# Kernel tuning notes

Measured on AMD Instinct MI355X. Metric: run time of the kernel, lower is better.

Reference implementation:

```python
import jax, jax.numpy as jnp
import numpy as np

N_NODES = 50000   # batch_size * num_nodes
N_EDGES = 800000
D_IN = 128
D_OUT = 128


def setup_inputs() -> dict:
    key = jax.random.key(0)
    k1, k2, k3, k4 = jax.random.split(key, 4)
    x = jax.random.normal(k1, (N_NODES, D_IN), dtype=jnp.float32)
    edge_index = jax.random.randint(k2, (2, N_EDGES), 0, N_NODES, dtype=jnp.int64)
    W = jax.random.normal(k3, (D_OUT, D_IN), dtype=jnp.float32) * (1.0 / np.sqrt(D_IN))
    b = jax.random.normal(k4, (D_OUT,), dtype=jnp.float32) * 0.01
    return {"x": x, "edge_index": edge_index, "batch_size": 50, "num_nodes": 1000, "W": W, "b": b}


def reference(x, edge_index, batch_size, num_nodes, W, b):
    dim_size = batch_size * num_nodes
    row, col = edge_index[0], edge_index[1]
    # gather messages and segment-mean aggregate over destination rows
    msgs = x[col]                                   # [E, D_IN]
    summed = jax.ops.segment_sum(msgs, row, num_segments=dim_size)      # [N, D_IN]
    counts = jax.ops.segment_sum(jnp.ones((row.shape[0],), dtype=x.dtype), row,
                                 num_segments=dim_size)                 # [N]
    mean = summed / jnp.maximum(counts, 1.0)[:, None]                   # 0 for empty rows
    # linear projection (torch Linear: y = x @ W.T + b)
    return mean @ W.T + b
```

## Files before the change

### kernel.cpp

```cpp
#include <hip/hip_runtime.h>

#define D 128
#define BSHIFT 5
#define BCAP 1024
#define EPB_A 2048

typedef unsigned short ushort_t;
typedef unsigned int uint_t;
typedef __attribute__((ext_vector_type(8))) short short8_t;
typedef __attribute__((ext_vector_type(4))) float f32x4_t;
typedef __attribute__((ext_vector_type(4))) uint_t uint4_t;
typedef const __attribute__((address_space(1))) void* gas_cptr;
typedef __attribute__((address_space(3))) void* las_ptr;
typedef const __attribute__((address_space(3))) ushort_t* las_cushort;

__device__ __forceinline__ bool eidx_is64(const int* eidx) {
    int lane = threadIdx.x & 63;
    int probe = eidx[2 * lane + 1];
    return __ballot(probe != 0) == 0ULL;
}

__device__ __forceinline__ uint_t f2bf(float f) {
    union { float f; uint_t i; } v; v.f = f;
    return (v.i + 0x7fffu + ((v.i >> 16) & 1u)) >> 16;
}
__device__ __forceinline__ float bf_lo(uint_t w) {
    union { uint_t i; float f; } v; v.i = w << 16; return v.f;
}
__device__ __forceinline__ float bf_hi(uint_t w) {
    union { uint_t i; float f; } v; v.i = w & 0xffff0000u; return v.f;
}

__global__ __launch_bounds__(256) void pre_kernel(
    const int* __restrict__ eidx, int* __restrict__ gcur,
    int* __restrict__ bucket, int E, int NBUK, int ab,
    const float* __restrict__ x, uint_t* __restrict__ xb, int total8, int cvb,
    const float* __restrict__ Wsrc, uint_t* __restrict__ wb, int N) {
    int t = threadIdx.x;

    if ((int)blockIdx.x >= ab) {
        if (xb == nullptr) return;
        int cb = blockIdx.x - ab;
        if (cb < cvb) {
            int i = cb * 256 + t;
            if (i < total8) {
                const float4* p = (const float4*)(x + (size_t)i * 8);
                float4 a = p[0], b = p[1];
                uint4 o;
                o.x = f2bf(a.x) | (f2bf(a.y) << 16);
                o.y = f2bf(a.z) | (f2bf(a.w) << 16);
                o.z = f2bf(b.x) | (f2bf(b.y) << 16);
                o.w = f2bf(b.z) | (f2bf(b.w) << 16);
                *(uint4*)(xb + (size_t)i * 4) = o;
            }
            if (cb == 0 && t < 16) {
                uint4 z; z.x = 0u; z.y = 0u; z.z = 0u; z.w = 0u;
                ((uint4*)(xb + (size_t)N * (D / 2)))[t] = z;
            }
        } else {
            int i = (cb - cvb) * 256 + t;
            if (i < D * D / 8) {
                const float4* p = (const float4*)(Wsrc + (size_t)i * 8);
                float4 a = p[0], b = p[1];
                uint4 o;
                o.x = f2bf(a.x) | (f2bf(a.y) << 16);
                o.y = f2bf(a.z) | (f2bf(a.w) << 16);
                o.z = f2bf(b.x) | (f2bf(b.y) << 16);
                o.w = f2bf(b.z) | (f2bf(b.w) << 16);
                *(uint4*)(wb + (size_t)i * 4) = o;
            }
        }
        return;
    }

    __shared__ int lhist[2048];
    __shared__ int lbase[2048];
    bool is64 = eidx_is64(eidx);
    for (int i = t; i < NBUK; i += 256) lhist[i] = 0;
    __syncthreads();

    int e0 = blockIdx.x * EPB_A;
    int e1 = min(e0 + EPB_A, E);
    int rr[8], cc[8];
    #pragma unroll
    for (int k = 0; k < 8; ++k) {
        int e = e0 + t + k * 256;
        rr[k] = -1;
        if (e < e1) {
            if (is64) { rr[k] = eidx[2 * e]; cc[k] = eidx[2 * E + 2 * e]; }
            else      { rr[k] = eidx[e];     cc[k] = eidx[E + e]; }
            atomicAdd(&lhist[rr[k] >> BSHIFT], 1);
        }
    }
    __syncthreads();
    for (int i = t; i < NBUK; i += 256) {
        int h = lhist[i];
        lbase[i] = (h > 0) ? atomicAdd(&gcur[i], h) : 0;
        lhist[i] = 0;
    }
    __syncthreads();
    #pragma unroll
    for (int k = 0; k < 8; ++k) {
        if (rr[k] >= 0) {
            int b = rr[k] >> BSHIFT;
            int p = atomicAdd(&lhist[b], 1);
            int idx = lbase[b] + p;
            if (idx < BCAP) bucket[b * BCAP + idx] = ((rr[k] & 31) << 24) | cc[k];
        }
    }
}

#define ISSUE(c, bufsel)                                                      \
    {                                                                         \
        ushort_t* db_ = wstage + (bufsel) * 2048;                             \
        __builtin_amdgcn_global_load_lds(                                     \
            (gas_cptr)(xb + (size_t)(c).x * D + 8 * sl),                      \
            (las_ptr)(db_), 16, 0, 0);                                        \
        __builtin_amdgcn_global_load_lds(                                     \
            (gas_cptr)(xb + (size_t)(c).y * D + 8 * sl),                      \
            (las_ptr)(db_ + 512), 16, 0, 0);                                  \
        __builtin_amdgcn_global_load_lds(                                     \
            (gas_cptr)(xb + (size_t)(c).z * D + 8 * sl),                      \
            (las_ptr)(db_ + 1024), 16, 0, 0);                                 \
        __builtin_amdgcn_global_load_lds(                                     \
            (gas_cptr)(xb + (size_t)(c).w * D + 8 * sl),                      \
            (las_ptr)(db_ + 1536), 16, 0, 0);                                 \
    }

#define ACCV(v)                                                               \
    a0 += bf_lo((v)[0]); a1 += bf_hi((v)[0]);                                 \
    a2 += bf_lo((v)[1]); a3 += bf_hi((v)[1]);                                 \
    a4 += bf_lo((v)[2]); a5 += bf_hi((v)[2]);                                 \
    a6 += bf_lo((v)[3]); a7 += bf_hi((v)[3]);

#define CONSUME                                                               \
    {                                                                         \
        uint4_t v0, v1, v2, v3;                                               \
        asm volatile("ds_read_b128 %0, %1"             : "=v"(v0) : "v"(sbp));\
        asm volatile("ds_read_b128 %0, %1 offset:1024" : "=v"(v1) : "v"(sbp));\
        asm volatile("ds_read_b128 %0, %1 offset:2048" : "=v"(v2) : "v"(sbp));\
        asm volatile("ds_read_b128 %0, %1 offset:3072" : "=v"(v3) : "v"(sbp));\
        asm volatile("s_waitcnt lgkmcnt(0)" ::: "memory");                    \
        __builtin_amdgcn_sched_barrier(0);                                    \
        ACCV(v0) ACCV(v1) ACCV(v2) ACCV(v3)                                   \
    }

__global__ __launch_bounds__(256, 3) void fused_bf_kernel(
    const ushort_t* __restrict__ xb, const int* __restrict__ gcur,
    const int* __restrict__ bucket, const ushort_t* __restrict__ Wb,
    const float* __restrict__ bias, float* __restrict__ out, int N) {
    __shared__ alignas(16) int sE[1152];
    __shared__ int lcnt[32], lpos[32], lstart[32];
    __shared__ alignas(16) ushort_t sA[32 * 136];
    __shared__ alignas(16) ushort_t stage[16384];
    int t = threadIdx.x;
    int b = blockIdx.x;

    if (t < 32) { lcnt[t] = 0; lpos[t] = 0; }
    __syncthreads();
    int tot = min(gcur[b], BCAP);
    const int* bp = bucket + (size_t)b * BCAP;
    for (int i = t; i < tot; i += 256)
        atomicAdd(&lcnt[bp[i] >> 24], 1);
    __syncthreads();
    if (t == 0) {
        int run = 0;
        #pragma unroll
        for (int i = 0; i < 32; ++i) {
            lstart[i] = run;
            run += (lcnt[i] + 3) & ~3;
        }
    }
    __syncthreads();
    for (int i = t; i < tot; i += 256) {
        int v = bp[i];
        int rl = v >> 24;
        int p = atomicAdd(&lpos[rl], 1);
        int idx = lstart[rl] + p;
        if (idx < 1152) sE[idx] = v & 0xFFFFFF;
    }
    if (t < 32) {
        int c0 = lcnt[t];
        int pe = (c0 + 3) & ~3;
        for (int p = c0; p < pe; ++p) {
            int idx = lstart[t] + p;
            if (idx < 1152) sE[idx] = N;
        }
    }
    __syncthreads();

    int lane = t & 63, wave = t >> 6;
    int qi = t >> 4, sl = t & 15;
    int nbase = b << BSHIFT;
    ushort_t* wstage = stage + (wave << 12);

    #pragma unroll
    for (int quad = 0; quad < 2; ++quad) {
        int n = 2 * qi + quad;
        int nr = lcnt[n];
        int st = lstart[n];
        int trips = ((nr + 3) & ~3) >> 2;
        int wmax = trips;
        wmax = max(wmax, __shfl_xor(wmax, 16));
        wmax = max(wmax, __shfl_xor(wmax, 32));
        float a0 = 0.f, a1 = 0.f, a2 = 0.f, a3 = 0.f;
        float a4 = 0.f, a5 = 0.f, a6 = 0.f, a7 = 0.f;
        if (wmax > 0) {
            int4 c0 = (0 < trips) ? *(const int4*)(sE + st)
                                  : make_int4(N, N, N, N);
            ISSUE(c0, 0)
            __builtin_amdgcn_sched_barrier(0);
            for (int bt = 0; bt < wmax; ++bt) {
                int buf = bt & 1;
                if (bt + 1 < wmax) {
                    int4 cn = (bt + 1 < trips)
                        ? *(const int4*)(sE + st + 4 * (bt + 1))
                        : make_int4(N, N, N, N);
                    ISSUE(cn, buf ^ 1)
                    __builtin_amdgcn_sched_barrier(0);
                    asm volatile("s_waitcnt vmcnt(4)" ::: "memory");
                } else {
                    asm volatile("s_waitcnt vmcnt(0)" ::: "memory");
                }
                __builtin_amdgcn_sched_barrier(0);
                las_cushort sbp = (las_cushort)(wstage + buf * 2048 + lane * 8);
                CONSUME
            }
        }
        float inv = (nr > 0) ? 1.0f / (float)nr : 0.0f;
        uint4 pk;
        pk.x = f2bf(a0 * inv) | (f2bf(a1 * inv) << 16);
        pk.y = f2bf(a2 * inv) | (f2bf(a3 * inv) << 16);
        pk.z = f2bf(a4 * inv) | (f2bf(a5 * inv) << 16);
        pk.w = f2bf(a6 * inv) | (f2bf(a7 * inv) << 16);
        *(uint4*)(sA + n * 136 + 8 * sl) = pk;
    }
    __syncthreads();

    {
        int rt = wave & 1, jgrp = wave >> 1;
        int ml = lane & 15, kh = lane >> 4;
        short8_t afr[4];
        #pragma unroll
        for (int ks = 0; ks < 4; ++ks)
            afr[ks] = *(const short8_t*)(sA + (rt * 16 + ml) * 136 + ks * 32 + kh * 8);
        f32x4_t acc[4];
        #pragma unroll
        for (int q = 0; q < 4; ++q) acc[q] = (f32x4_t){0.f, 0.f, 0.f, 0.f};
        #pragma unroll
        for (int q = 0; q < 4; ++q) {
            int j = (jgrp * 4 + q) * 16 + ml;
            #pragma unroll
            for (int ks = 0; ks < 4; ++ks) {
                short8_t bfr = *(const short8_t*)(Wb + (size_t)j * D + ks * 32 + kh * 8);
                acc[q] = __builtin_amdgcn_mfma_f32_16x16x32_bf16(afr[ks], bfr, acc[q], 0, 0, 0);
            }
        }
        #pragma unroll
        for (int q = 0; q < 4; ++q) {
            int j = (jgrp * 4 + q) * 16 + ml;
            float bj = bias[j];
            #pragma unroll
            for (int r = 0; r < 4; ++r) {
                int gn = nbase + rt * 16 + kh * 4 + r;
                if (gn < N) out[(size_t)gn * D + j] = acc[q][r] + bj;
            }
        }
    }
}

__global__ __launch_bounds__(256) void prep_kernel(
    const int* __restrict__ gcur, const int* __restrict__ bucket,
    int* __restrict__ elist, int* __restrict__ cnt,
    int* __restrict__ start, int N, int NBUK) {
    __shared__ int lcnt[32], lpos[32], lstart[32];
    int t = threadIdx.x;
    int b = blockIdx.x;
    if (t < 32) { lcnt[t] = 0; lpos[t] = 0; }
    __syncthreads();
    int tot = min(gcur[b], BCAP);
    const int* bp = bucket + (size_t)b * BCAP;
    for (int i = t; i < tot; i += 256)
        atomicAdd(&lcnt[bp[i] >> 24], 1);
    __syncthreads();
    if (t == 0) {
        int run = 0;
        #pragma unroll
        for (int i = 0; i < 32; ++i) {
            lstart[i] = run;
            run += (lcnt[i] + 3) & ~3;
        }
    }
    __syncthreads();
    for (int i = t; i < tot; i += 256) {
        int v = bp[i];
        int rl = v >> 24;
        int p = atomicAdd(&lpos[rl], 1);
        int idx = lstart[rl] + p;
        if (idx < BCAP) elist[(size_t)b * BCAP + idx] = v & 0xFFFFFF;
    }
    if (t < 32) {
        int gr = (b << BSHIFT) + t;
        if (gr < N) { cnt[gr] = lcnt[t]; start[gr] = b * BCAP + lstart[t]; }
    }
}

__global__ __launch_bounds__(256, 6) void fused_kernel(
    const float* __restrict__ x, const int* __restrict__ elist,
    const int* __restrict__ cnt, const int* __restrict__ start,
    const float* __restrict__ W, const float* __restrict__ bias,
    float* __restrict__ out, int N) {
    __shared__ float sT[128 * 36];
    __shared__ float wc[16 * 132];
    int t = threadIdx.x;
    int lane = t & 63, wave = t >> 6;
    int half = lane >> 5, sl = lane & 31;
    int nbase = blockIdx.x * 32;

    #pragma unroll
    for (int pair = 0; pair < 4; ++pair) {
        int n = wave * 8 + pair * 2 + half;
        int gn = nbase + n;
        int nr  = (gn < N) ? cnt[gn]   : 0;
        int beg = (gn < N) ? start[gn] : 0;
        int nro  = __shfl(nr, lane ^ 32);
        int both = min(nr, nro);
        float ax = 0.f, ay = 0.f, az = 0.f, aw = 0.f;
        int i = 0;
        for (; i + 8 <= both; i += 8) {
            int4 cA = *(const int4*)(elist + beg + i);
            int4 cB = *(const int4*)(elist + beg + i + 4);
            float4 v0 = *(const float4*)(x + (size_t)cA.x * D + 4 * sl);
            float4 v1 = *(const float4*)(x + (size_t)cA.y * D + 4 * sl);
            float4 v2 = *(const float4*)(x + (size_t)cA.z * D + 4 * sl);
            float4 v3 = *(const float4*)(x + (size_t)cA.w * D + 4 * sl);
            float4 v4 = *(const float4*)(x + (size_t)cB.x * D + 4 * sl);
            float4 v5 = *(const float4*)(x + (size_t)cB.y * D + 4 * sl);
            float4 v6 = *(const float4*)(x + (size_t)cB.z * D + 4 * sl);
            float4 v7 = *(const float4*)(x + (size_t)cB.w * D + 4 * sl);
            ax += ((v0.x + v1.x) + (v2.x + v3.x)) + ((v4.x + v5.x) + (v6.x + v7.x));
            ay += ((v0.y + v1.y) + (v2.y + v3.y)) + ((v4.y + v5.y) + (v6.y + v7.y));
            az += ((v0.z + v1.z) + (v2.z + v3.z)) + ((v4.z + v5.z) + (v6.z + v7.z));
            aw += ((v0.w + v1.w) + (v2.w + v3.w)) + ((v4.w + v5.w) + (v6.w + v7.w));
        }
        for (; i < nr; ++i) {
            int c0 = elist[beg + i];
            float4 v = *(const float4*)(x + (size_t)c0 * D + 4 * sl);
            ax += v.x; ay += v.y; az += v.z; aw += v.w;
        }
        float inv = (nr > 0) ? 1.0f / (float)nr : 0.0f;
        int k0 = 4 * sl;
        sT[(k0 + 0) * 36 + n] = ax * inv;
        sT[(k0 + 1) * 36 + n] = ay * inv;
        sT[(k0 + 2) * 36 + n] = az * inv;
        sT[(k0 + 3) * 36 + n] = aw * inv;
    }

    int jg = t & 31, ng = t >> 5;
    int j0 = jg * 4, n0 = ng * 4;
    float acc[4][4] = {};
    for (int kc = 0; kc < 8; ++kc) {
        __syncthreads();
        #pragma unroll
        for (int i = 0; i < 8; ++i) {
            int idx = t + i * 256;
            int j = idx >> 4, kk = idx & 15;
            wc[kk * 132 + j] = W[j * D + kc * 16 + kk];
        }
        __syncthreads();
        #pragma unroll
        for (int kk = 0; kk < 16; ++kk) {
            int k = kc * 16 + kk;
            float4 s4 = *(const float4*)(sT + k * 36 + n0);
            float4 w4 = *(const float4*)(wc + kk * 132 + j0);
            acc[0][0] = fmaf(s4.x, w4.x, acc[0][0]); acc[0][1] = fmaf(s4.x, w4.y, acc[0][1]);
            acc[0][2] = fmaf(s4.x, w4.z, acc[0][2]); acc[0][3] = fmaf(s4.x, w4.w, acc[0][3]);
            acc[1][0] = fmaf(s4.y, w4.x, acc[1][0]); acc[1][1] = fmaf(s4.y, w4.y, acc[1][1]);
            acc[1][2] = fmaf(s4.y, w4.z, acc[1][2]); acc[1][3] = fmaf(s4.y, w4.w, acc[1][3]);
            acc[2][0] = fmaf(s4.z, w4.x, acc[2][0]); acc[2][1] = fmaf(s4.z, w4.y, acc[2][1]);
            acc[2][2] = fmaf(s4.z, w4.z, acc[2][2]); acc[2][3] = fmaf(s4.z, w4.w, acc[2][3]);
            acc[3][0] = fmaf(s4.w, w4.x, acc[3][0]); acc[3][1] = fmaf(s4.w, w4.y, acc[3][1]);
            acc[3][2] = fmaf(s4.w, w4.z, acc[3][2]); acc[3][3] = fmaf(s4.w, w4.w, acc[3][3]);
        }
    }
    float4 b4 = *(const float4*)(bias + j0);
    #pragma unroll
    for (int i = 0; i < 4; ++i) {
        int gn = nbase + n0 + i;
        if (gn >= N) continue;
        float4 o;
        o.x = acc[i][0] + b4.x;
        o.y = acc[i][1] + b4.y;
        o.z = acc[i][2] + b4.z;
        o.w = acc[i][3] + b4.w;
        *(float4*)(out + (size_t)gn * D + j0) = o;
    }
}

__global__ __launch_bounds__(256) void scatter_kernel(
    const float* __restrict__ x, const int* __restrict__ eidx,
    float* summed, float* __restrict__ counts, int E) {
    int t = blockIdx.x * 256 + threadIdx.x;
    int lane = threadIdx.x & 63;
    bool is64 = eidx_is64(eidx);
    int e = t >> 6;
    if (e >= E) return;
    int d = lane * 2;
    int r, c;
    if (is64) { r = eidx[2 * e]; c = eidx[2 * E + 2 * e]; }
    else      { r = eidx[e];     c = eidx[E + e]; }
    float2 v = *(const float2*)(x + (size_t)c * D + d);
    float* dst = summed + (size_t)r * D + d;
    atomicAdd(dst, v.x);
    atomicAdd(dst + 1, v.y);
    if (lane == 0) atomicAdd(counts + r, 1.0f);
}

__global__ __launch_bounds__(256) void divide_kernel(
    float* __restrict__ sums, const float* __restrict__ counts, int N) {
    int g = blockIdx.x * 256 + threadIdx.x;
    int r = g >> 6, lane = g & 63;
    if (r >= N) return;
    float inv = 1.0f / fmaxf(counts[r], 1.0f);
    float2* p = (float2*)(sums + (size_t)r * D + 2 * lane);
    float2 v = *p;
    v.x *= inv; v.y *= inv;
    *p = v;
}

__global__ __launch_bounds__(256) void gemm_kernel(
    float* inout, const float* __restrict__ W,
    const float* __restrict__ bias, int N) {
    __shared__ float sT[128 * 36];
    __shared__ float wc[32 * 132];
    int t = threadIdx.x;
    int nbase = blockIdx.x * 32;
    #pragma unroll
    for (int i = 0; i < 16; ++i) {
        int idx = t + i * 256;
        int n = idx >> 7, k = idx & 127;
        int gn = nbase + n;
        sT[k * 36 + n] = (gn < N) ? inout[(size_t)gn * D + k] : 0.0f;
    }
    int jg = t & 31, ng = t >> 5;
    int j0 = jg * 4, n0 = ng * 4;
    float acc[4][4] = {};
    for (int kc = 0; kc < 4; ++kc) {
        __syncthreads();
        #pragma unroll
        for (int i = 0; i < 16; ++i) {
            int idx = t + i * 256;
            int j = idx >> 5, kk = idx & 31;
            wc[kk * 132 + j] = W[j * D + kc * 32 + kk];
        }
        __syncthreads();
        #pragma unroll 8
        for (int kk = 0; kk < 32; ++kk) {
            int k = kc * 32 + kk;
            float4 s4 = *(const float4*)(sT + k * 36 + n0);
            float4 w4 = *(const float4*)(wc + kk * 132 + j0);
            acc[0][0] = fmaf(s4.x, w4.x, acc[0][0]); acc[0][1] = fmaf(s4.x, w4.y, acc[0][1]);
            acc[0][2] = fmaf(s4.x, w4.z, acc[0][2]); acc[0][3] = fmaf(s4.x, w4.w, acc[0][3]);
            acc[1][0] = fmaf(s4.y, w4.x, acc[1][0]); acc[1][1] = fmaf(s4.y, w4.y, acc[1][1]);
            acc[1][2] = fmaf(s4.y, w4.z, acc[1][2]); acc[1][3] = fmaf(s4.y, w4.w, acc[1][3]);
            acc[2][0] = fmaf(s4.z, w4.x, acc[2][0]); acc[2][1] = fmaf(s4.z, w4.y, acc[2][1]);
            acc[2][2] = fmaf(s4.z, w4.z, acc[2][2]); acc[2][3] = fmaf(s4.z, w4.w, acc[2][3]);
            acc[3][0] = fmaf(s4.w, w4.x, acc[3][0]); acc[3][1] = fmaf(s4.w, w4.y, acc[3][1]);
            acc[3][2] = fmaf(s4.w, w4.z, acc[3][2]); acc[3][3] = fmaf(s4.w, w4.w, acc[3][3]);
        }
    }
    float4 b4 = *(const float4*)(bias + j0);
    #pragma unroll
    for (int i = 0; i < 4; ++i) {
        int gn = nbase + n0 + i;
        if (gn >= N) continue;
        float4 o;
        o.x = acc[i][0] + b4.x;
        o.y = acc[i][1] + b4.y;
        o.z = acc[i][2] + b4.z;
        o.w = acc[i][3] + b4.w;
        *(float4*)(inout + (size_t)gn * D + j0) = o;
    }
}

extern "C" void kernel_launch(void* const* d_in, const int* in_sizes, int n_in,
                              void* d_out, int out_size, void* d_ws, size_t ws_size,
                              hipStream_t stream) {
    const float* x = (const float*)d_in[0];
    const int* eidx = (const int*)d_in[1];
    const float* W = (const float*)d_in[4];
    const float* b = (const float*)d_in[5];
    float* out = (float*)d_out;

    int N = in_sizes[0] / D;
    int E = in_sizes[1] / 2;
    int NBUK = (N + 31) >> BSHIFT;
    int ab = (E + EPB_A - 1) / EPB_A;

    size_t o0 = 0;
    size_t o_gc = o0;  o0 += ((size_t)NBUK * 4 + 255) & ~255ULL;
    size_t o_cn = o0;  o0 += ((size_t)N * 4 + 255) & ~255ULL;
    size_t o_st = o0;  o0 += ((size_t)N * 4 + 255) & ~255ULL;
    size_t o_bk = o0;  o0 += (size_t)NBUK * BCAP * 4;
    size_t o_el = o0;  o0 += (size_t)NBUK * BCAP * 4;
    size_t base_need = o0;
    size_t o_xb = o0;  o0 += (((size_t)(N + 1) * D * 2) + 255) & ~255ULL;
    size_t o_wb = o0;  size_t bf_need = o0 + (size_t)D * D * 2;

    bool cap_ok = (N <= 65536) && ((size_t)NBUK * BCAP >= (size_t)E);

    int cvb = (N * D / 8 + 255) / 256;
    int wvb = (D * D / 8 + 255) / 256;

    if (cap_ok && ws_size >= bf_need) {
        char* ws = (char*)d_ws;
        int*      gcur  = (int*)(ws + o_gc);
        int*      bkt   = (int*)(ws + o_bk);
        ushort_t* xb    = (ushort_t*)(ws + o_xb);
        ushort_t* wb    = (ushort_t*)(ws + o_wb);

        hipMemsetAsync(gcur, 0, (size_t)NBUK * 4, stream);
        pre_kernel<<<ab + cvb + wvb, 256, 0, stream>>>(
            eidx, gcur, bkt, E, NBUK, ab,
            x, (uint_t*)xb, N * D / 8, cvb, W, (uint_t*)wb, N);
        fused_bf_kernel<<<NBUK, 256, 0, stream>>>(xb, gcur, bkt, wb, b, out, N);
    } else if (cap_ok && ws_size >= base_need) {
        char* ws = (char*)d_ws;
        int* gcur  = (int*)(ws + o_gc);
        int* cnt   = (int*)(ws + o_cn);
        int* start = (int*)(ws + o_st);
        int* bkt   = (int*)(ws + o_bk);
        int* elist = (int*)(ws + o_el);
        int fb = (N + 31) / 32;

        hipMemsetAsync(gcur, 0, (size_t)NBUK * 4, stream);
        pre_kernel<<<ab, 256, 0, stream>>>(
            eidx, gcur, bkt, E, NBUK, ab,
            nullptr, nullptr, 0, 0, nullptr, nullptr, N);
        prep_kernel<<<NBUK, 256, 0, stream>>>(gcur, bkt, elist, cnt, start, N, NBUK);
        fused_kernel<<<fb, 256, 0, stream>>>(x, elist, cnt, start, W, b, out, N);
    } else {
        float* counts = (float*)d_ws;
        int fb = (N + 31) / 32;
        hipMemsetAsync(d_out, 0, (size_t)N * D * sizeof(float), stream);
        hipMemsetAsync(d_ws, 0, (size_t)N * sizeof(float), stream);
        int sb = (E * 64 + 255) / 256;
        scatter_kernel<<<sb, 256, 0, stream>>>(x, eidx, out, counts, E);
        int db = (N * 64 + 255) / 256;
        divide_kernel<<<db, 256, 0, stream>>>(out, counts, N);
        gemm_kernel<<<fb, 256, 0, stream>>>(out, W, b, N);
    }
}
```

Baseline: 157.8 us.

## Merge bucketing/convert and aggregate+GEMM into one persistent kernel with grid barrier

Replaces the two-kernel sequence (bucketing plus bf16 conversion, then fused aggregate+GEMM) with a single persistent kernel of fixed grid size. Blocks first loop over the bucketing and conversion tasks, then meet at a software grid barrier built on a global atomic counter, then loop over node buckets for the aggregation and MFMA projection. This removes one kernel launch and the gap between kernels, at the cost of a spin-wait barrier that needs all 768 blocks resident at once, plus the loss of the natural one-block-per-bucket scheduling.

```diff
diff --git a/kernel.cpp b/kernel.cpp
--- a/kernel.cpp
+++ b/kernel.cpp
@@ -4,6 +4,7 @@
 #define BSHIFT 5
 #define BCAP 1024
 #define EPB_A 2048
+#define GRID_MONO 768
 
 typedef unsigned short ushort_t;
 typedef unsigned int uint_t;
@@ -31,84 +32,6 @@
     union { uint_t i; float f; } v; v.i = w & 0xffff0000u; return v.f;
 }
 
-__global__ __launch_bounds__(256) void pre_kernel(
-    const int* __restrict__ eidx, int* __restrict__ gcur,
-    int* __restrict__ bucket, int E, int NBUK, int ab,
-    const float* __restrict__ x, uint_t* __restrict__ xb, int total8, int cvb,
-    const float* __restrict__ Wsrc, uint_t* __restrict__ wb, int N) {
-    int t = threadIdx.x;
-
-    if ((int)blockIdx.x >= ab) {
-        if (xb == nullptr) return;
-        int cb = blockIdx.x - ab;
-        if (cb < cvb) {
-            int i = cb * 256 + t;
-            if (i < total8) {
-                const float4* p = (const float4*)(x + (size_t)i * 8);
-                float4 a = p[0], b = p[1];
-                uint4 o;
-                o.x = f2bf(a.x) | (f2bf(a.y) << 16);
-                o.y = f2bf(a.z) | (f2bf(a.w) << 16);
-                o.z = f2bf(b.x) | (f2bf(b.y) << 16);
-                o.w = f2bf(b.z) | (f2bf(b.w) << 16);
-                *(uint4*)(xb + (size_t)i * 4) = o;
-            }
-            if (cb == 0 && t < 16) {
-                uint4 z; z.x = 0u; z.y = 0u; z.z = 0u; z.w = 0u;
-                ((uint4*)(xb + (size_t)N * (D / 2)))[t] = z;
-            }
-        } else {
-            int i = (cb - cvb) * 256 + t;
-            if (i < D * D / 8) {
-                const float4* p = (const float4*)(Wsrc + (size_t)i * 8);
-                float4 a = p[0], b = p[1];
-                uint4 o;
-                o.x = f2bf(a.x) | (f2bf(a.y) << 16);
-                o.y = f2bf(a.z) | (f2bf(a.w) << 16);
-                o.z = f2bf(b.x) | (f2bf(b.y) << 16);
-                o.w = f2bf(b.z) | (f2bf(b.w) << 16);
-                *(uint4*)(wb + (size_t)i * 4) = o;
-            }
-        }
-        return;
-    }
-
-    __shared__ int lhist[2048];
-    __shared__ int lbase[2048];
-    bool is64 = eidx_is64(eidx);
-    for (int i = t; i < NBUK; i += 256) lhist[i] = 0;
-    __syncthreads();
-
-    int e0 = blockIdx.x * EPB_A;
-    int e1 = min(e0 + EPB_A, E);
-    int rr[8], cc[8];
-    #pragma unroll
-    for (int k = 0; k < 8; ++k) {
-        int e = e0 + t + k * 256;
-        rr[k] = -1;
-        if (e < e1) {
-            if (is64) { rr[k] = eidx[2 * e]; cc[k] = eidx[2 * E + 2 * e]; }
-            else      { rr[k] = eidx[e];     cc[k] = eidx[E + e]; }
-            atomicAdd(&lhist[rr[k] >> BSHIFT], 1);
-        }
-    }
-    __syncthreads();
-    for (int i = t; i < NBUK; i += 256) {
-        int h = lhist[i];
-        lbase[i] = (h > 0) ? atomicAdd(&gcur[i], h) : 0;
-        lhist[i] = 0;
-    }
-    __syncthreads();
-    #pragma unroll
-    for (int k = 0; k < 8; ++k) {
-        if (rr[k] >= 0) {
-            int b = rr[k] >> BSHIFT;
-            int p = atomicAdd(&lhist[b], 1);
-            int idx = lbase[b] + p;
-            if (idx < BCAP) bucket[b * BCAP + idx] = ((rr[k] & 31) << 24) | cc[k];
-        }
-    }
-}
 
 #define ISSUE(c, bufsel)                                                      \
     {                                                                         \
@@ -145,126 +68,251 @@
         ACCV(v0) ACCV(v1) ACCV(v2) ACCV(v3)                                   \
     }
 
-__global__ __launch_bounds__(256, 3) void fused_bf_kernel(
-    const ushort_t* __restrict__ xb, const int* __restrict__ gcur,
-    const int* __restrict__ bucket, const ushort_t* __restrict__ Wb,
-    const float* __restrict__ bias, float* __restrict__ out, int N) {
+__global__ __launch_bounds__(256, 3) void mono_kernel(
+    const int* __restrict__ eidx, int* __restrict__ gcur,
+    int* __restrict__ bucket, const float* __restrict__ x,
+    ushort_t* __restrict__ xb, const float* __restrict__ Wsrc,
+    ushort_t* __restrict__ wb, const float* __restrict__ bias,
+    float* __restrict__ out, uint_t* __restrict__ bar,
+    int E, int N, int NBUK, int ab, int cvb, int wvb, int total8) {
+    __shared__ alignas(16) ushort_t stage[16384];
     __shared__ alignas(16) int sE[1152];
     __shared__ int lcnt[32], lpos[32], lstart[32];
     __shared__ alignas(16) ushort_t sA[32 * 136];
-    __shared__ alignas(16) ushort_t stage[16384];
     int t = threadIdx.x;
-    int b = blockIdx.x;
-
-    if (t < 32) { lcnt[t] = 0; lpos[t] = 0; }
-    __syncthreads();
-    int tot = min(gcur[b], BCAP);
-    const int* bp = bucket + (size_t)b * BCAP;
-    for (int i = t; i < tot; i += 256)
-        atomicAdd(&lcnt[bp[i] >> 24], 1);
+
+    int* lhist = (int*)stage;
+    int* lbase = (int*)(stage + 4096);
+    int ntask = ab + cvb + wvb;
+    for (int vt = blockIdx.x; vt < ntask; vt += gridDim.x) {
+        if (vt < ab) {
+            bool is64 = eidx_is64(eidx);
+            for (int i = t; i < NBUK; i += 256) lhist[i] = 0;
+            __syncthreads();
+            int e0 = vt * EPB_A;
+            int e1 = min(e0 + EPB_A, E);
+            int rr[8], cc[8];
+            #pragma unroll
+            for (int k = 0; k < 8; ++k) {
+                int e = e0 + t + k * 256;
+                rr[k] = -1;
+                if (e < e1) {
+                    if (is64) { rr[k] = eidx[2 * e]; cc[k] = eidx[2 * E + 2 * e]; }
+                    else      { rr[k] = eidx[e];     cc[k] = eidx[E + e]; }
+                    atomicAdd(&lhist[rr[k] >> BSHIFT], 1);
+                }
+            }
+            __syncthreads();
+            for (int i = t; i < NBUK; i += 256) {
+                int h = lhist[i];
+                lbase[i] = (h > 0) ? atomicAdd(&gcur[i], h) : 0;
+                lhist[i] = 0;
+            }
+            __syncthreads();
+            #pragma unroll
+            for (int k = 0; k < 8; ++k) {
+                if (rr[k] >= 0) {
+                    int b = rr[k] >> BSHIFT;
+                    int p = atomicAdd(&lhist[b], 1);
+                    int idx = lbase[b] + p;
+                    if (idx < BCAP) bucket[b * BCAP + idx] = ((rr[k] & 31) << 24) | cc[k];
+                }
+            }
+            __syncthreads();
+        } else if (vt < ab + cvb) {
+            int cb = vt - ab;
+            int i = cb * 256 + t;
+            if (i < total8) {
+                const float4* p = (const float4*)(x + (size_t)i * 8);
+                float4 a = p[0], b = p[1];
+                uint4 o;
+                o.x = f2bf(a.x) | (f2bf(a.y) << 16);
+                o.y = f2bf(a.z) | (f2bf(a.w) << 16);
+                o.z = f2bf(b.x) | (f2bf(b.y) << 16);
+                o.w = f2bf(b.z) | (f2bf(b.w) << 16);
+                *(uint4*)((uint_t*)xb + (size_t)i * 4) = o;
+            }
+            if (cb == 0 && t < 16) {
+                uint4 z; z.x = 0u; z.y = 0u; z.z = 0u; z.w = 0u;
+                ((uint4*)(xb + (size_t)N * D))[t] = z;
+            }
+        } else {
+            int i = (vt - ab - cvb) * 256 + t;
+            if (i < D * D / 8) {
+                const float4* p = (const float4*)(Wsrc + (size_t)i * 8);
+                float4 a = p[0], b = p[1];
+                uint4 o;
+                o.x = f2bf(a.x) | (f2bf(a.y) << 16);
+                o.y = f2bf(a.z) | (f2bf(a.w) << 16);
+                o.z = f2bf(b.x) | (f2bf(b.y) << 16);
+                o.w = f2bf(b.z) | (f2bf(b.w) << 16);
+                *(uint4*)((uint_t*)wb + (size_t)i * 4) = o;
+            }
+        }
+    }
+
+    __threadfence();
     __syncthreads();
     if (t == 0) {
-        int run = 0;
-        #pragma unroll
-        for (int i = 0; i < 32; ++i) {
-            lstart[i] = run;
-            run += (lcnt[i] + 3) & ~3;
-        }
-    }
-    __syncthreads();
-    for (int i = t; i < tot; i += 256) {
-        int v = bp[i];
-        int rl = v >> 24;
-        int p = atomicAdd(&lpos[rl], 1);
-        int idx = lstart[rl] + p;
-        if (idx < 1152) sE[idx] = v & 0xFFFFFF;
-    }
-    if (t < 32) {
-        int c0 = lcnt[t];
-        int pe = (c0 + 3) & ~3;
-        for (int p = c0; p < pe; ++p) {
-            int idx = lstart[t] + p;
-            if (idx < 1152) sE[idx] = N;
-        }
+        __hip_atomic_fetch_add(bar, 1u, __ATOMIC_RELEASE, __HIP_MEMORY_SCOPE_AGENT);
+        while (__hip_atomic_load(bar, __ATOMIC_ACQUIRE, __HIP_MEMORY_SCOPE_AGENT)
+               < (uint_t)gridDim.x)
+            __builtin_amdgcn_s_sleep(8);
     }
     __syncthreads();
 
     int lane = t & 63, wave = t >> 6;
     int qi = t >> 4, sl = t & 15;
-    int nbase = b << BSHIFT;
     ushort_t* wstage = stage + (wave << 12);
-
+    const ushort_t* Wb = wb;
+
+    for (int buk = blockIdx.x; buk < NBUK; buk += gridDim.x) {
+        if (t < 32) { lcnt[t] = 0; lpos[t] = 0; }
+        __syncthreads();
+        int tot = min(gcur[buk], BCAP);
+        const int* bp = bucket + (size_t)buk * BCAP;
+        for (int i = t; i < tot; i += 256)
+            atomicAdd(&lcnt[bp[i] >> 24], 1);
+        __syncthreads();
+        if (t == 0) {
+            int run = 0;
+            #pragma unroll
+            for (int i = 0; i < 32; ++i) {
+                lstart[i] = run;
+                run += (lcnt[i] + 3) & ~3;
+            }
+        }
+        __syncthreads();
+        for (int i = t; i < tot; i += 256) {
+            int v = bp[i];
+            int rl = v >> 24;
+            int p = atomicAdd(&lpos[rl], 1);
+            int idx = lstart[rl] + p;
+            if (idx < 1152) sE[idx] = v & 0xFFFFFF;
+        }
+        if (t < 32) {
+            int c0 = lcnt[t];
+            int pe = (c0 + 3) & ~3;
+            for (int p = c0; p < pe; ++p) {
+                int idx = lstart[t] + p;
+                if (idx < 1152) sE[idx] = N;
+            }
+        }
+        __syncthreads();
+
+        int nbase = buk << BSHIFT;
+        #pragma unroll
+        for (int quad = 0; quad < 2; ++quad) {
+            int n = 2 * qi + quad;
+            int nr = lcnt[n];
+            int st = lstart[n];
+            int trips = ((nr + 3) & ~3) >> 2;
+            int wmax = trips;
+            wmax = max(wmax, __shfl_xor(wmax, 16));
+            wmax = max(wmax, __shfl_xor(wmax, 32));
+            float a0 = 0.f, a1 = 0.f, a2 = 0.f, a3 = 0.f;
+            float a4 = 0.f, a5 = 0.f, a6 = 0.f, a7 = 0.f;
+            if (wmax > 0) {
+                int4 c0 = (0 < trips) ? *(const int4*)(sE + st)
+                                      : make_int4(N, N, N, N);
+                ISSUE(c0, 0)
+                __builtin_amdgcn_sched_barrier(0);
+                for (int bt = 0; bt < wmax; ++bt) {
+                    int buf = bt & 1;
+                    if (bt + 1 < wmax) {
+                        int4 cn = (bt + 1 < trips)
+                            ? *(const int4*)(sE + st + 4 * (bt + 1))
+                            : make_int4(N, N, N, N);
+                        ISSUE(cn, buf ^ 1)
+                        __builtin_amdgcn_sched_barrier(0);
+                        asm volatile("s_waitcnt vmcnt(4)" ::: "memory");
+                    } else {
+                        asm volatile("s_waitcnt vmcnt(0)" ::: "memory");
+                    }
+                    __builtin_amdgcn_sched_barrier(0);
+                    las_cushort sbp = (las_cushort)(wstage + buf * 2048 + lane * 8);
+                    CONSUME
+                }
+            }
+            float inv = (nr > 0) ? 1.0f / (float)nr : 0.0f;
+            uint4 pk;
+            pk.x = f2bf(a0 * inv) | (f2bf(a1 * inv) << 16);
+            pk.y = f2bf(a2 * inv) | (f2bf(a3 * inv) << 16);
+            pk.z = f2bf(a4 * inv) | (f2bf(a5 * inv) << 16);
+            pk.w = f2bf(a6 * inv) | (f2bf(a7 * inv) << 16);
+            *(uint4*)(sA + n * 136 + 8 * sl) = pk;
+        }
+        __syncthreads();
+
+        {
+            int rt = wave & 1, jgrp = wave >> 1;
+            int ml = lane & 15, kh = lane >> 4;
+            short8_t afr[4];
+            #pragma unroll
+            for (int ks = 0; ks < 4; ++ks)
+                afr[ks] = *(const short8_t*)(sA + (rt * 16 + ml) * 136 + ks * 32 + kh * 8);
+            f32x4_t acc[4];
+            #pragma unroll
+            for (int q = 0; q < 4; ++q) acc[q] = (f32x4_t){0.f, 0.f, 0.f, 0.f};
+            #pragma unroll
+            for (int q = 0; q < 4; ++q) {
+                int j = (jgrp * 4 + q) * 16 + ml;
+                #pragma unroll
+                for (int ks = 0; ks < 4; ++ks) {
+                    short8_t bfr = *(const short8_t*)(Wb + (size_t)j * D + ks * 32 + kh * 8);
+                    acc[q] = __builtin_amdgcn_mfma_f32_16x16x32_bf16(afr[ks], bfr, acc[q], 0, 0, 0);
+                }
+            }
+            #pragma unroll
+            for (int q = 0; q < 4; ++q) {
+                int j = (jgrp * 4 + q) * 16 + ml;
+                float bj = bias[j];
+                #pragma unroll
+                for (int r = 0; r < 4; ++r) {
+                    int gn = nbase + rt * 16 + kh * 4 + r;
+                    if (gn < N) out[(size_t)gn * D + j] = acc[q][r] + bj;
+                }
+            }
+        }
+    }
+}
+
+__global__ __launch_bounds__(256) void pre_kernel(
+    const int* __restrict__ eidx, int* __restrict__ gcur,
+    int* __restrict__ bucket, int E, int NBUK) {
+    __shared__ int lhist[2048];
+    __shared__ int lbase[2048];
+    bool is64 = eidx_is64(eidx);
+    int t = threadIdx.x;
+    for (int i = t; i < NBUK; i += 256) lhist[i] = 0;
+    __syncthreads();
+    int e0 = blockIdx.x * EPB_A;
+    int e1 = min(e0 + EPB_A, E);
+    int rr[8], cc[8];
     #pragma unroll
-    for (int quad = 0; quad < 2; ++quad) {
-        int n = 2 * qi + quad;
-        int nr = lcnt[n];
-        int st = lstart[n];
-        int trips = ((nr + 3) & ~3) >> 2;
-        int wmax = trips;
-        wmax = max(wmax, __shfl_xor(wmax, 16));
-        wmax = max(wmax, __shfl_xor(wmax, 32));
-        float a0 = 0.f, a1 = 0.f, a2 = 0.f, a3 = 0.f;
-        float a4 = 0.f, a5 = 0.f, a6 = 0.f, a7 = 0.f;
-        if (wmax > 0) {
-            int4 c0 = (0 < trips) ? *(const int4*)(sE + st)
-                                  : make_int4(N, N, N, N);
-            ISSUE(c0, 0)
-            __builtin_amdgcn_sched_barrier(0);
-            for (int bt = 0; bt < wmax; ++bt) {
-                int buf = bt & 1;
-                if (bt + 1 < wmax) {
-                    int4 cn = (bt + 1 < trips)
-                        ? *(const int4*)(sE + st + 4 * (bt + 1))
-                        : make_int4(N, N, N, N);
-                    ISSUE(cn, buf ^ 1)
-                    __builtin_amdgcn_sched_barrier(0);
-                    asm volatile("s_waitcnt vmcnt(4)" ::: "memory");
-                } else {
-                    asm volatile("s_waitcnt vmcnt(0)" ::: "memory");
-                }
-                __builtin_amdgcn_sched_barrier(0);
-                las_cushort sbp = (las_cushort)(wstage + buf * 2048 + lane * 8);
-                CONSUME
-            }
-        }
-        float inv = (nr > 0) ? 1.0f / (float)nr : 0.0f;
-        uint4 pk;
-        pk.x = f2bf(a0 * inv) | (f2bf(a1 * inv) << 16);
-        pk.y = f2bf(a2 * inv) | (f2bf(a3 * inv) << 16);
-        pk.z = f2bf(a4 * inv) | (f2bf(a5 * inv) << 16);
-        pk.w = f2bf(a6 * inv) | (f2bf(a7 * inv) << 16);
-        *(uint4*)(sA + n * 136 + 8 * sl) = pk;
-    }
-    __syncthreads();
-
-    {
-        int rt = wave & 1, jgrp = wave >> 1;
-        int ml = lane & 15, kh = lane >> 4;
-        short8_t afr[4];
-        #pragma unroll
-        for (int ks = 0; ks < 4; ++ks)
-            afr[ks] = *(const short8_t*)(sA + (rt * 16 + ml) * 136 + ks * 32 + kh * 8);
-        f32x4_t acc[4];
-        #pragma unroll
-        for (int q = 0; q < 4; ++q) acc[q] = (f32x4_t){0.f, 0.f, 0.f, 0.f};
-        #pragma unroll
-        for (int q = 0; q < 4; ++q) {
-            int j = (jgrp * 4 + q) * 16 + ml;
-            #pragma unroll
-            for (int ks = 0; ks < 4; ++ks) {
-                short8_t bfr = *(const short8_t*)(Wb + (size_t)j * D + ks * 32 + kh * 8);
-                acc[q] = __builtin_amdgcn_mfma_f32_16x16x32_bf16(afr[ks], bfr, acc[q], 0, 0, 0);
-            }
-        }
-        #pragma unroll
-        for (int q = 0; q < 4; ++q) {
-            int j = (jgrp * 4 + q) * 16 + ml;
-            float bj = bias[j];
-            #pragma unroll
-            for (int r = 0; r < 4; ++r) {
-                int gn = nbase + rt * 16 + kh * 4 + r;
-                if (gn < N) out[(size_t)gn * D + j] = acc[q][r] + bj;
-            }
+    for (int k = 0; k < 8; ++k) {
+        int e = e0 + t + k * 256;
+        rr[k] = -1;
+        if (e < e1) {
+            if (is64) { rr[k] = eidx[2 * e]; cc[k] = eidx[2 * E + 2 * e]; }
+            else      { rr[k] = eidx[e];     cc[k] = eidx[E + e]; }
+            atomicAdd(&lhist[rr[k] >> BSHIFT], 1);
+        }
+    }
+    __syncthreads();
+    for (int i = t; i < NBUK; i += 256) {
+        int h = lhist[i];
+        lbase[i] = (h > 0) ? atomicAdd(&gcur[i], h) : 0;
+        lhist[i] = 0;
+    }
+    __syncthreads();
+    #pragma unroll
+    for (int k = 0; k < 8; ++k) {
+        if (rr[k] >= 0) {
+            int b = rr[k] >> BSHIFT;
+            int p = atomicAdd(&lhist[b], 1);
+            int idx = lbase[b] + p;
+            if (idx < BCAP) bucket[b * BCAP + idx] = ((rr[k] & 31) << 24) | cc[k];
         }
     }
 }
@@ -498,7 +546,7 @@
     int ab = (E + EPB_A - 1) / EPB_A;
 
     size_t o0 = 0;
-    size_t o_gc = o0;  o0 += ((size_t)NBUK * 4 + 255) & ~255ULL;
+    size_t o_gc = o0;  o0 += ((size_t)NBUK * 4 + 4 + 255) & ~255ULL;
     size_t o_cn = o0;  o0 += ((size_t)N * 4 + 255) & ~255ULL;
     size_t o_st = o0;  o0 += ((size_t)N * 4 + 255) & ~255ULL;
     size_t o_bk = o0;  o0 += (size_t)NBUK * BCAP * 4;
@@ -515,15 +563,15 @@
     if (cap_ok && ws_size >= bf_need) {
         char* ws = (char*)d_ws;
         int*      gcur  = (int*)(ws + o_gc);
+        uint_t*   bar   = (uint_t*)(ws + o_gc + (size_t)NBUK * 4);
         int*      bkt   = (int*)(ws + o_bk);
         ushort_t* xb    = (ushort_t*)(ws + o_xb);
         ushort_t* wb    = (ushort_t*)(ws + o_wb);
 
-        hipMemsetAsync(gcur, 0, (size_t)NBUK * 4, stream);
-        pre_kernel<<<ab + cvb + wvb, 256, 0, stream>>>(
-            eidx, gcur, bkt, E, NBUK, ab,
-            x, (uint_t*)xb, N * D / 8, cvb, W, (uint_t*)wb, N);
-        fused_bf_kernel<<<NBUK, 256, 0, stream>>>(xb, gcur, bkt, wb, b, out, N);
+        hipMemsetAsync(gcur, 0, (size_t)NBUK * 4 + 4, stream);
+        mono_kernel<<<GRID_MONO, 256, 0, stream>>>(
+            eidx, gcur, bkt, x, xb, W, wb, b, out, bar,
+            E, N, NBUK, ab, cvb, wvb, N * D / 8);
     } else if (cap_ok && ws_size >= base_need) {
         char* ws = (char*)d_ws;
         int* gcur  = (int*)(ws + o_gc);
@@ -534,9 +582,7 @@
         int fb = (N + 31) / 32;
 
         hipMemsetAsync(gcur, 0, (size_t)NBUK * 4, stream);
-        pre_kernel<<<ab, 256, 0, stream>>>(
-            eidx, gcur, bkt, E, NBUK, ab,
-            nullptr, nullptr, 0, 0, nullptr, nullptr, N);
+        pre_kernel<<<ab, 256, 0, stream>>>(eidx, gcur, bkt, E, NBUK);
         prep_kernel<<<NBUK, 256, 0, stream>>>(gcur, bkt, elist, cnt, start, N, NBUK);
         fused_kernel<<<fb, 256, 0, stream>>>(x, elist, cnt, start, W, b, out, N);
     } else {
```

After: 370.2 us. 135% more time.

## Triple-buffer gather staging and vectorize edge/bucket index loads

Applied to the files above, without the earlier changes.

Extends the per-wave LDS staging used for the neighbour gather from a double buffer to a triple buffer, so two batches of row loads stay in flight while one is accumulated. The added LDS lowers the occupancy target from 3 to 2 blocks per CU. The bucketing pass now loads each thread's 8 contiguous edge indices with int4 loads instead of strided scalar loads. The fused kernel reads its bucket entries once with a vector load into registers, then reuses them for both the count and scatter passes. Giving up occupancy for deeper prefetch may not pay off if latency was already hidden.

```diff
diff --git a/kernel.cpp b/kernel.cpp
--- a/kernel.cpp
+++ b/kernel.cpp
@@ -81,17 +81,47 @@
 
     int e0 = blockIdx.x * EPB_A;
     int e1 = min(e0 + EPB_A, E);
+    int base = e0 + 8 * t;
     int rr[8], cc[8];
     #pragma unroll
-    for (int k = 0; k < 8; ++k) {
-        int e = e0 + t + k * 256;
-        rr[k] = -1;
-        if (e < e1) {
-            if (is64) { rr[k] = eidx[2 * e]; cc[k] = eidx[2 * E + 2 * e]; }
-            else      { rr[k] = eidx[e];     cc[k] = eidx[E + e]; }
-            atomicAdd(&lhist[rr[k] >> BSHIFT], 1);
-        }
-    }
+    for (int k = 0; k < 8; ++k) rr[k] = -1;
+    if (is64) {
+        if (base + 8 <= e1 && (E & 1) == 0) {
+            const int4* rp = (const int4*)(eidx + 2 * (size_t)base);
+            const int4* cp = (const int4*)(eidx + 2 * (size_t)E + 2 * (size_t)base);
+            #pragma unroll
+            for (int g = 0; g < 4; ++g) {
+                int4 r = rp[g], c = cp[g];
+                rr[2 * g]     = r.x; cc[2 * g]     = c.x;
+                rr[2 * g + 1] = r.z; cc[2 * g + 1] = c.z;
+            }
+        } else {
+            #pragma unroll
+            for (int k = 0; k < 8; ++k) {
+                int e = base + k;
+                if (e < e1) { rr[k] = eidx[2 * e]; cc[k] = eidx[2 * E + 2 * e]; }
+            }
+        }
+    } else {
+        if (base + 8 <= e1 && (E & 3) == 0) {
+            const int4* rp = (const int4*)(eidx + base);
+            const int4* cp = (const int4*)(eidx + (size_t)E + base);
+            int4 r0 = rp[0], r1 = rp[1], c0 = cp[0], c1 = cp[1];
+            rr[0] = r0.x; rr[1] = r0.y; rr[2] = r0.z; rr[3] = r0.w;
+            rr[4] = r1.x; rr[5] = r1.y; rr[6] = r1.z; rr[7] = r1.w;
+            cc[0] = c0.x; cc[1] = c0.y; cc[2] = c0.z; cc[3] = c0.w;
+            cc[4] = c1.x; cc[5] = c1.y; cc[6] = c1.z; cc[7] = c1.w;
+        } else {
+            #pragma unroll
+            for (int k = 0; k < 8; ++k) {
+                int e = base + k;
+                if (e < e1) { rr[k] = eidx[e]; cc[k] = eidx[E + e]; }
+            }
+        }
+    }
+    #pragma unroll
+    for (int k = 0; k < 8; ++k)
+        if (rr[k] >= 0) atomicAdd(&lhist[rr[k] >> BSHIFT], 1);
     __syncthreads();
     for (int i = t; i < NBUK; i += 256) {
         int h = lhist[i];
@@ -145,14 +175,14 @@
         ACCV(v0) ACCV(v1) ACCV(v2) ACCV(v3)                                   \
     }
 
-__global__ __launch_bounds__(256, 3) void fused_bf_kernel(
+__global__ __launch_bounds__(256, 2) void fused_bf_kernel(
     const ushort_t* __restrict__ xb, const int* __restrict__ gcur,
     const int* __restrict__ bucket, const ushort_t* __restrict__ Wb,
     const float* __restrict__ bias, float* __restrict__ out, int N) {
     __shared__ alignas(16) int sE[1152];
     __shared__ int lcnt[32], lpos[32], lstart[32];
     __shared__ alignas(16) ushort_t sA[32 * 136];
-    __shared__ alignas(16) ushort_t stage[16384];
+    __shared__ alignas(16) ushort_t stage[24576];
     int t = threadIdx.x;
     int b = blockIdx.x;
 
@@ -160,8 +190,19 @@
     __syncthreads();
     int tot = min(gcur[b], BCAP);
     const int* bp = bucket + (size_t)b * BCAP;
-    for (int i = t; i < tot; i += 256)
-        atomicAdd(&lcnt[bp[i] >> 24], 1);
+    int4 ev = make_int4(-1, -1, -1, -1);
+    if (4 * t + 3 < tot) {
+        ev = *(const int4*)(bp + 4 * t);
+    } else {
+        if (4 * t + 0 < tot) ev.x = bp[4 * t + 0];
+        if (4 * t + 1 < tot) ev.y = bp[4 * t + 1];
+        if (4 * t + 2 < tot) ev.z = bp[4 * t + 2];
+        if (4 * t + 3 < tot) ev.w = bp[4 * t + 3];
+    }
+    if (ev.x >= 0) atomicAdd(&lcnt[ev.x >> 24], 1);
+    if (ev.y >= 0) atomicAdd(&lcnt[ev.y >> 24], 1);
+    if (ev.z >= 0) atomicAdd(&lcnt[ev.z >> 24], 1);
+    if (ev.w >= 0) atomicAdd(&lcnt[ev.w >> 24], 1);
     __syncthreads();
     if (t == 0) {
         int run = 0;
@@ -172,12 +213,17 @@
         }
     }
     __syncthreads();
-    for (int i = t; i < tot; i += 256) {
-        int v = bp[i];
-        int rl = v >> 24;
-        int p = atomicAdd(&lpos[rl], 1);
-        int idx = lstart[rl] + p;
-        if (idx < 1152) sE[idx] = v & 0xFFFFFF;
+    {
+        int v[4] = { ev.x, ev.y, ev.z, ev.w };
+        #pragma unroll
+        for (int q = 0; q < 4; ++q) {
+            if (v[q] >= 0) {
+                int rl = v[q] >> 24;
+                int p = atomicAdd(&lpos[rl], 1);
+                int idx = lstart[rl] + p;
+                if (idx < 1152) sE[idx] = v[q] & 0xFFFFFF;
+            }
+        }
     }
     if (t < 32) {
         int c0 = lcnt[t];
@@ -192,7 +238,7 @@
     int lane = t & 63, wave = t >> 6;
     int qi = t >> 4, sl = t & 15;
     int nbase = b << BSHIFT;
-    ushort_t* wstage = stage + (wave << 12);
+    ushort_t* wstage = stage + wave * 6144;
 
     #pragma unroll
     for (int quad = 0; quad < 2; ++quad) {
@@ -206,25 +252,34 @@
         float a0 = 0.f, a1 = 0.f, a2 = 0.f, a3 = 0.f;
         float a4 = 0.f, a5 = 0.f, a6 = 0.f, a7 = 0.f;
         if (wmax > 0) {
-            int4 c0 = (0 < trips) ? *(const int4*)(sE + st)
-                                  : make_int4(N, N, N, N);
-            ISSUE(c0, 0)
+            int4 cc0 = (0 < trips) ? *(const int4*)(sE + st)
+                                   : make_int4(N, N, N, N);
+            ISSUE(cc0, 0)
+            if (wmax > 1) {
+                int4 cc1 = (1 < trips) ? *(const int4*)(sE + st + 4)
+                                       : make_int4(N, N, N, N);
+                ISSUE(cc1, 1)
+            }
             __builtin_amdgcn_sched_barrier(0);
+            int bsel = 0;
             for (int bt = 0; bt < wmax; ++bt) {
-                int buf = bt & 1;
-                if (bt + 1 < wmax) {
-                    int4 cn = (bt + 1 < trips)
-                        ? *(const int4*)(sE + st + 4 * (bt + 1))
+                if (bt + 2 < wmax) {
+                    int nb = bsel + 2; if (nb >= 3) nb -= 3;
+                    int4 cn = (bt + 2 < trips)
+                        ? *(const int4*)(sE + st + 4 * (bt + 2))
                         : make_int4(N, N, N, N);
-                    ISSUE(cn, buf ^ 1)
+                    ISSUE(cn, nb)
                     __builtin_amdgcn_sched_barrier(0);
+                    asm volatile("s_waitcnt vmcnt(8)" ::: "memory");
+                } else if (bt + 1 < wmax) {
                     asm volatile("s_waitcnt vmcnt(4)" ::: "memory");
                 } else {
                     asm volatile("s_waitcnt vmcnt(0)" ::: "memory");
                 }
                 __builtin_amdgcn_sched_barrier(0);
-                las_cushort sbp = (las_cushort)(wstage + buf * 2048 + lane * 8);
+                las_cushort sbp = (las_cushort)(wstage + bsel * 2048 + lane * 8);
                 CONSUME
+                bsel = (bsel == 2) ? 0 : bsel + 1;
             }
         }
         float inv = (nr > 0) ? 1.0f / (float)nr : 0.0f;
```

Result: slower. 161.0 us (+2.1%).
